# Kernel tuning notes

Measured on AMD Instinct MI355X. Metric: run time of the kernel, lower is better.

Reference implementation:

```python
import jax, jax.numpy as jnp
import numpy as np

N = 100000
E = 800000

def elu(x):
    return jnp.where(x > 0, x, jnp.expm1(x))

def transformer_conv(x, src, dst, ea, Wq, bq, Wk, bk, Wv, bv, We, Ws, bs, heads, ch):
    # PyG TransformerConv (concat=True, root_weight=True, beta=False, eval so dropout off)
    n = x.shape[0]
    q = (x @ Wq + bq).reshape(n, heads, ch)
    k = (x @ Wk + bk).reshape(n, heads, ch)
    v = (x @ Wv + bv).reshape(n, heads, ch)
    e = (ea @ We).reshape(-1, heads, ch)            # [E,H,C], lin_edge has no bias
    kj = k[src] + e                                  # [E,H,C]
    logits = (q[dst] * kj).sum(-1) / jnp.sqrt(jnp.float32(ch))  # [E,H]
    # segment softmax over incoming edges of each dst node
    m = jax.ops.segment_max(logits, dst, num_segments=n)
    ex = jnp.exp(logits - m[dst])
    denom = jax.ops.segment_sum(ex, dst, num_segments=n)
    alpha = ex / denom[dst]                          # [E,H]
    msg = alpha[..., None] * (v[src] + e)            # [E,H,C]
    agg = jax.ops.segment_sum(msg, dst, num_segments=n).reshape(n, heads * ch)
    return agg + x @ Ws + bs                         # skip connection (lin_skip)

def setup_inputs() -> dict:
    key = jax.random.key(0)
    ks = jax.random.split(key, 32)
    def rn(k, shape, scale=0.1):
        return jax.random.normal(k, shape, dtype=jnp.float32) * scale
    d = {}
    d['x'] = jax.random.normal(ks[0], (N, 23), dtype=jnp.float32)
    d['edge_index'] = jax.random.randint(ks[1], (2, E), 0, N, dtype=jnp.int32)
    d['edge_attr'] = jax.random.normal(ks[2], (E, 7), dtype=jnp.float32)
    d['linA_w'] = rn(ks[3], (23, 23)); d['linA_b'] = jnp.zeros((23,), jnp.float32)
    d['linB_w'] = rn(ks[4], (23, 23)); d['linB_b'] = jnp.zeros((23,), jnp.float32)
    # conv1: in=23, heads=8, out=24 -> 192
    d['q1_w'] = rn(ks[5], (23, 192)); d['q1_b'] = jnp.zeros((192,), jnp.float32)
    d['k1_w'] = rn(ks[6], (23, 192)); d['k1_b'] = jnp.zeros((192,), jnp.float32)
    d['v1_w'] = rn(ks[7], (23, 192)); d['v1_b'] = jnp.zeros((192,), jnp.float32)
    d['e1_w'] = rn(ks[8], (7, 192))
    d['s1_w'] = rn(ks[9], (23, 192)); d['s1_b'] = jnp.zeros((192,), jnp.float32)
    # conv4: in=192, heads=8, out=8 -> 64
    d['q2_w'] = rn(ks[10], (192, 64)); d['q2_b'] = jnp.zeros((64,), jnp.float32)
    d['k2_w'] = rn(ks[11], (192, 64)); d['k2_b'] = jnp.zeros((64,), jnp.float32)
    d['v2_w'] = rn(ks[12], (192, 64)); d['v2_b'] = jnp.zeros((64,), jnp.float32)
    d['e2_w'] = rn(ks[13], (7, 64))
    d['s2_w'] = rn(ks[14], (192, 64)); d['s2_b'] = jnp.zeros((64,), jnp.float32)
    d['lin1_w'] = rn(ks[15], (64, 20)); d['lin1_b'] = jnp.zeros((20,), jnp.float32)
    d['lin2_w'] = rn(ks[16], (20, 1)); d['lin2_b'] = jnp.zeros((1,), jnp.float32)
    return d

def reference(x, edge_index, edge_attr,
              linA_w, linA_b, linB_w, linB_b,
              q1_w, q1_b, k1_w, k1_b, v1_w, v1_b, e1_w, s1_w, s1_b,
              q2_w, q2_b, k2_w, k2_b, v2_w, v2_b, e2_w, s2_w, s2_b,
              lin1_w, lin1_b, lin2_w, lin2_b):
    src, dst = edge_index[0], edge_index[1]
    h = elu(x @ linA_w + linA_b)
    h = elu(h @ linB_w + linB_b)
    h = transformer_conv(h, src, dst, edge_attr, q1_w, q1_b, k1_w, k1_b, v1_w, v1_b, e1_w, s1_w, s1_b, 8, 24)
    h = elu(h)
    h = transformer_conv(h, src, dst, edge_attr, q2_w, q2_b, k2_w, k2_b, v2_w, v2_b, e2_w, s2_w, s2_b, 8, 8)
    h = elu(h)
    h = elu(h @ lin1_w + lin1_b)
    return h @ lin2_w + lin2_b
```

## Files before the change

### kernel.cpp

```cpp
#include <hip/hip_runtime.h>
#include <math.h>


__device__ __forceinline__ float elu_f(float x) {
    return x > 0.f ? x : expm1f(x);
}


__global__ void mlp_kernel(const float* __restrict__ x,
                           const float* __restrict__ A, const float* __restrict__ ab,
                           const float* __restrict__ B, const float* __restrict__ bb,
                           float* __restrict__ out, int n) {
    __shared__ float sA[23 * 23], sB[23 * 23], sa[23], sb[23];
    for (int t = threadIdx.x; t < 23 * 23; t += blockDim.x) { sA[t] = A[t]; sB[t] = B[t]; }
    if (threadIdx.x < 23) { sa[threadIdx.x] = ab[threadIdx.x]; sb[threadIdx.x] = bb[threadIdx.x]; }
    __syncthreads();
    int i = blockIdx.x * blockDim.x + threadIdx.x;
    if (i >= n) return;
    float xi[23], h1[23];
    #pragma unroll
    for (int j = 0; j < 23; j++) xi[j] = x[(size_t)i * 23 + j];
    #pragma unroll
    for (int o = 0; o < 23; o++) {
        float acc = sa[o];
        #pragma unroll
        for (int j = 0; j < 23; j++) acc = fmaf(xi[j], sA[j * 23 + o], acc);
        h1[o] = elu_f(acc);
    }
    #pragma unroll
    for (int o = 0; o < 23; o++) {
        float acc = sb[o];
        #pragma unroll
        for (int j = 0; j < 23; j++) acc = fmaf(h1[j], sB[j * 23 + o], acc);
        out[(size_t)i * 23 + o] = elu_f(acc);
    }
}

template<int IN, int Kc, int OUTW, int M, int TY>
__global__ void proj_tiled_kernel(const float* __restrict__ in, int n,
    const float* __restrict__ W0, const float* __restrict__ b0, float* __restrict__ o0,
    const float* __restrict__ W1, const float* __restrict__ b1, float* __restrict__ o1,
    const float* __restrict__ W2, const float* __restrict__ b2, float* __restrict__ o2,
    const float* __restrict__ W3, const float* __restrict__ b3, float* __restrict__ o3) {
    constexpr int WTOT = M * OUTW;
    constexpr int CG   = WTOT / 8;
    constexpr int BN   = TY * 4;
    constexpr int SAW  = BN + 4;
    constexpr int NT   = CG * TY;
    static_assert(IN % Kc == 0, "Kc must divide IN");
    static_assert(WTOT % 8 == 0 && OUTW % 4 == 0, "col alignment");
    __shared__ float sA[Kc][SAW];
    __shared__ float sB[Kc][WTOT];

    const int tid = threadIdx.x;
    const int tx = tid % CG;
    const int ty = tid / CG;
    const int node0 = blockIdx.x * BN;

    const int colA = tx * 4;
    const int colB = WTOT / 2 + tx * 4;
    const int matA = colA / OUTW, ccA = colA % OUTW;
    const int matB = colB / OUTW, ccB = colB % OUTW;
    const float* bA = (matA == 0 ? b0 : matA == 1 ? b1 : matA == 2 ? b2 : b3);
    const float* bB = (matB == 0 ? b0 : matB == 1 ? b1 : matB == 2 ? b2 : b3);
    float*       oA = (matA == 0 ? o0 : matA == 1 ? o1 : matA == 2 ? o2 : o3);
    float*       oB = (matB == 0 ? o0 : matB == 1 ? o1 : matB == 2 ? o2 : o3);

    float acc[4][8];
    #pragma unroll
    for (int i = 0; i < 4; i++) {
        #pragma unroll
        for (int c = 0; c < 4; c++) { acc[i][c] = bA[ccA + c]; acc[i][4 + c] = bB[ccB + c]; }
    }

    for (int k0 = 0; k0 < IN; k0 += Kc) {
        for (int t = tid; t < Kc * BN; t += NT) {
            int j = t / BN, nn = t - j * BN;
            int g = node0 + nn;
            sA[j][nn] = (g < n) ? in[(size_t)g * IN + k0 + j] : 0.f;
        }
        for (int t = tid; t < Kc * WTOT; t += NT) {
            int j = t / WTOT, c = t - j * WTOT;
            int m = c / OUTW, cm = c - m * OUTW;
            const float* Wp = (m == 0 ? W0 : m == 1 ? W1 : m == 2 ? W2 : W3);
            sB[j][c] = Wp[(size_t)(k0 + j) * OUTW + cm];
        }
        __syncthreads();
        #pragma unroll 8
        for (int j = 0; j < Kc; j++) {
            float4 a  = *(const float4*)&sA[j][ty * 4];
            float4 v0 = *(const float4*)&sB[j][colA];
            float4 v1 = *(const float4*)&sB[j][colB];
            float av[4] = {a.x, a.y, a.z, a.w};
            float bv[8] = {v0.x, v0.y, v0.z, v0.w, v1.x, v1.y, v1.z, v1.w};
            #pragma unroll
            for (int i = 0; i < 4; i++)
                #pragma unroll
                for (int c = 0; c < 8; c++)
                    acc[i][c] = fmaf(av[i], bv[c], acc[i][c]);
        }
        __syncthreads();
    }

    #pragma unroll
    for (int i = 0; i < 4; i++) {
        int g = node0 + ty * 4 + i;
        if (g >= n) continue;
        *(float4*)(oA + (size_t)g * OUTW + ccA) = make_float4(acc[i][0], acc[i][1], acc[i][2], acc[i][3]);
        *(float4*)(oB + (size_t)g * OUTW + ccB) = make_float4(acc[i][4], acc[i][5], acc[i][6], acc[i][7]);
    }
}


__global__ void zero2_kernel(int* __restrict__ a, int* __restrict__ b, int n) {
    int i = blockIdx.x * blockDim.x + threadIdx.x;
    if (i < n) { a[i] = 0; b[i] = 0; }
}

__global__ void count_kernel(const int* __restrict__ dst, int* __restrict__ cnt, int nE) {
    int e = blockIdx.x * blockDim.x + threadIdx.x;
    if (e < nE) atomicAdd(&cnt[dst[e]], 1);
}

__global__ void scan_block_kernel(int* __restrict__ cnt, int* __restrict__ bsum, int n) {
    __shared__ int sdat[256];
    int i = blockIdx.x * 256 + threadIdx.x;
    int v = (i < n) ? cnt[i] : 0;
    sdat[threadIdx.x] = v;
    __syncthreads();
    for (int off = 1; off < 256; off <<= 1) {
        int t = (threadIdx.x >= (unsigned)off) ? sdat[threadIdx.x - off] : 0;
        __syncthreads();
        sdat[threadIdx.x] += t;
        __syncthreads();
    }
    if (i < n) cnt[i] = sdat[threadIdx.x] - v;
    if (threadIdx.x == 255) bsum[blockIdx.x] = sdat[255];
}

__global__ void scan_bsum_kernel(int* __restrict__ bsum, int nb) {
    __shared__ int s[1024];
    int i = threadIdx.x;
    int v = (i < nb) ? bsum[i] : 0;
    s[i] = v;
    __syncthreads();
    for (int off = 1; off < 1024; off <<= 1) {
        int t = (i >= off) ? s[i - off] : 0;
        __syncthreads();
        s[i] += t;
        __syncthreads();
    }
    if (i < nb) bsum[i] = s[i] - v;
}

__global__ void finalize_rp_kernel(const int* __restrict__ cnt, const int* __restrict__ bsum,
                                   int* __restrict__ rp, int n, int nE) {
    int i = blockIdx.x * blockDim.x + threadIdx.x;
    if (i < n) rp[i] = cnt[i] + bsum[i >> 8];
    if (i == n) rp[n] = nE;
}

__global__ void scatter_kernel(const int* __restrict__ src, const int* __restrict__ dst,
                               const int* __restrict__ rp, int* __restrict__ cur,
                               int* __restrict__ srcS, int* __restrict__ eidS, int nE) {
    int e = blockIdx.x * blockDim.x + threadIdx.x;
    if (e >= nE) return;
    int d = dst[e];
    int pos = rp[d] + atomicAdd(&cur[d], 1);
    srcS[pos] = src[e];
    eidS[pos] = e;
}

template<int IN, int C, bool VMAT, bool QMAT, bool DOELU>
__global__ void conv_fused_kernel(const float* __restrict__ feat,
                                  const float* __restrict__ Wq, const float* __restrict__ qb,
                                  const float* __restrict__ Wv, const float* __restrict__ vb,
                                  const float* __restrict__ kmat, const float* __restrict__ vmat,
                                  const float* __restrict__ qmat,
                                  const float* __restrict__ ea, const float* __restrict__ We,
                                  const int* __restrict__ rp, const int* __restrict__ srcS,
                                  const int* __restrict__ eidS,
                                  float* __restrict__ out, int n, float scale) {
    constexpr int HC = 8 * C;
    constexpr int CPL = HC / 64;
    __shared__ float sWv[VMAT ? 1 : IN * HC];
    if constexpr (!VMAT) {
        for (int t = threadIdx.x; t < IN * HC; t += blockDim.x) sWv[t] = Wv[t];
        __syncthreads();
    }
    const int lane = threadIdx.x & 63;
    const int d = blockIdx.x * (blockDim.x >> 6) + (threadIdx.x >> 6);
    if (d >= n) return;
    const int ch0 = lane * CPL;

    float we[7][CPL];
    #pragma unroll
    for (int j = 0; j < 7; j++)
        #pragma unroll
        for (int c = 0; c < CPL; c++) we[j][c] = We[j * HC + ch0 + c];

    float vbr[CPL];
    if constexpr (!VMAT) {
        #pragma unroll
        for (int c = 0; c < CPL; c++) vbr[c] = vb[ch0 + c];
    }

    float* op = out + (size_t)d * HC + ch0;
    float sk[CPL], q[CPL];
    #pragma unroll
    for (int c = 0; c < CPL; c++) sk[c] = op[c];
    if constexpr (QMAT) {
        const float* qp = qmat + (size_t)d * HC + ch0;
        #pragma unroll
        for (int c = 0; c < CPL; c++) q[c] = qp[c];
    } else {
        #pragma unroll
        for (int c = 0; c < CPL; c++) q[c] = qb[ch0 + c];
        const float* fd = feat + (size_t)d * IN;
        for (int j = 0; j < IN; j++) {
            float f = fd[j];
            #pragma unroll
            for (int c = 0; c < CPL; c++)
                q[c] = fmaf(f, Wq[(size_t)j * HC + ch0 + c], q[c]);
        }
    }

    float m = -INFINITY, l = 0.f, acc[CPL];
    #pragma unroll
    for (int c = 0; c < CPL; c++) acc[c] = 0.f;

    const int p0 = rp[d], p1 = rp[d + 1];
    for (int p = p0; p < p1; p++) {
        int s = srcS[p];
        int eid = eidS[p];
        const float* eav = ea + (size_t)eid * 7;
        float ev[7];
        #pragma unroll
        for (int j = 0; j < 7; j++) ev[j] = eav[j];

        const float* kp = kmat + (size_t)s * HC + ch0;
        float vv[CPL];
        float part = 0.f;
        #pragma unroll
        for (int c = 0; c < CPL; c++) {
            float ec = 0.f;
            #pragma unroll
            for (int j = 0; j < 7; j++) ec = fmaf(ev[j], we[j][c], ec);
            part = fmaf(q[c], kp[c] + ec, part);
            vv[c] = ec;
        }
        if constexpr (VMAT) {
            const float* vp = vmat + (size_t)s * HC + ch0;
            #pragma unroll
            for (int c = 0; c < CPL; c++) vv[c] += vp[c];
        } else {
            #pragma unroll
            for (int c = 0; c < CPL; c++) vv[c] += vbr[c];
            const float* fs = feat + (size_t)s * IN;
            for (int j = 0; j < IN; j++) {
                float f = fs[j];
                #pragma unroll
                for (int c = 0; c < CPL; c++) vv[c] = fmaf(f, sWv[j * HC + ch0 + c], vv[c]);
            }
        }
        part += __shfl_xor(part, 1);
        part += __shfl_xor(part, 2);
        part += __shfl_xor(part, 4);
        float z = part * scale;
        float mn = fmaxf(m, z);
        float rs = expf(m - mn);
        float pw = expf(z - mn);
        l = l * rs + pw;
        #pragma unroll
        for (int c = 0; c < CPL; c++) acc[c] = fmaf(acc[c], rs, pw * vv[c]);
        m = mn;
    }
    float invl = (l > 0.f) ? 1.f / l : 0.f;
    #pragma unroll
    for (int c = 0; c < CPL; c++) {
        float r = sk[c] + acc[c] * invl;
        op[c] = DOELU ? elu_f(r) : r;
    }
}

__global__ void head_kernel(const float* __restrict__ h, const float* __restrict__ W1,
                            const float* __restrict__ b1, const float* __restrict__ W2,
                            const float* __restrict__ b2, float* __restrict__ out, int n) {
    __shared__ float sW1[64 * 20], sb1[20], sW2[20], sb2;
    for (int t = threadIdx.x; t < 64 * 20; t += blockDim.x) sW1[t] = W1[t];
    if (threadIdx.x < 20) { sb1[threadIdx.x] = b1[threadIdx.x]; sW2[threadIdx.x] = W2[threadIdx.x]; }
    if (threadIdx.x == 0) sb2 = b2[0];
    __syncthreads();
    int i = blockIdx.x * blockDim.x + threadIdx.x;
    if (i >= n) return;
    float hv[64];
    const float* hp = h + (size_t)i * 64;
    #pragma unroll
    for (int j = 0; j < 64; j++) hv[j] = elu_f(hp[j]);
    float acc2 = sb2;
    for (int o = 0; o < 20; o++) {
        float a = sb1[o];
        #pragma unroll
        for (int j = 0; j < 64; j++) a = fmaf(hv[j], sW1[j * 20 + o], a);
        acc2 = fmaf(elu_f(a), sW2[o], acc2);
    }
    out[i] = acc2;
}

__global__ void zero_out_kernel(float* __restrict__ out, int n) {
    int i = blockIdx.x * blockDim.x + threadIdx.x;
    if (i < n) out[i] = 0.f;
}


extern "C" void kernel_launch(void* const* d_in, const int* in_sizes, int n_in,
                              void* d_out, int out_size, void* d_ws, size_t ws_size,
                              hipStream_t stream) {
    const float* x   = (const float*)d_in[0];
    const int*   ei  = (const int*)d_in[1];
    const float* ea  = (const float*)d_in[2];
    const float* Aw  = (const float*)d_in[3];
    const float* Ab  = (const float*)d_in[4];
    const float* Bw  = (const float*)d_in[5];
    const float* Bb  = (const float*)d_in[6];
    const float* q1w = (const float*)d_in[7];  const float* q1b = (const float*)d_in[8];
    const float* k1w = (const float*)d_in[9];  const float* k1b = (const float*)d_in[10];
    const float* v1w = (const float*)d_in[11]; const float* v1b = (const float*)d_in[12];
    const float* e1w = (const float*)d_in[13];
    const float* s1w = (const float*)d_in[14]; const float* s1b = (const float*)d_in[15];
    const float* q2w = (const float*)d_in[16]; const float* q2b = (const float*)d_in[17];
    const float* k2w = (const float*)d_in[18]; const float* k2b = (const float*)d_in[19];
    const float* v2w = (const float*)d_in[20]; const float* v2b = (const float*)d_in[21];
    const float* e2w = (const float*)d_in[22];
    const float* s2w = (const float*)d_in[23]; const float* s2b = (const float*)d_in[24];
    const float* l1w = (const float*)d_in[25]; const float* l1b = (const float*)d_in[26];
    const float* l2w = (const float*)d_in[27]; const float* l2b = (const float*)d_in[28];

    const int n  = in_sizes[0] / 23;
    const int nE = in_sizes[1] / 2;
    const int* src = ei;
    const int* dst = ei + nE;
    float* out = (float*)d_out;
    const int B = 256;
    const int nb = (n + 255) / 256;

    size_t fl_h1 = ((size_t)n * 23 + 3) & ~(size_t)3;
    size_t fl_o1 = (size_t)n * 192;
    size_t fl_kvA = (size_t)n * 384;
    size_t fl_kB  = (size_t)n * 192;
    size_t ints_total = ((size_t)n + 1) + n + n + 1024 + (size_t)nE + (size_t)nE;

    size_t tierA_bytes = (fl_h1 + fl_o1 + fl_kvA) * 4 + ints_total * 4;
    size_t tierB_bytes = (fl_h1 + fl_o1 + fl_kB) * 4 + ints_total * 4;

    if (ws_size < tierB_bytes || nb > 1024) {
        zero_out_kernel<<<(out_size + B - 1) / B, B, 0, stream>>>(out, out_size);
        return;
    }
    const bool tierA = (ws_size >= tierA_bytes);

    float* ws = (float*)d_ws;
    size_t off = 0;
    float* h1   = ws + off; off += fl_h1;
    float* o1   = ws + off; off += fl_o1;
    float* kbuf = ws + off; off += (tierA ? fl_kvA : fl_kB);
    float* vbuf = tierA ? (kbuf + (size_t)n * 192) : nullptr;
    int* ip = (int*)(ws + off);
    int* rp   = ip; ip += (size_t)n + 1;
    int* cnt  = ip; ip += n;
    int* cur  = ip; ip += n;
    int* bsum = ip; ip += 1024;
    int* srcS = ip; ip += nE;
    int* eidS = ip; ip += nE;

    float* q2buf = kbuf;
    float* k2    = tierA ? (kbuf + (size_t)n * 64)  : kbuf;
    float* v2    = tierA ? (kbuf + (size_t)n * 128) : (kbuf + (size_t)n * 64);
    float* o2    = tierA ? (kbuf + (size_t)n * 192) : (kbuf + (size_t)n * 128);

    const float sc1 = 1.0f / sqrtf(24.0f);
    const float sc2 = 1.0f / sqrtf(8.0f);
    const float* np = nullptr;
    float* npw = nullptr;

    zero2_kernel<<<(n + B - 1) / B, B, 0, stream>>>(cnt, cur, n);
    count_kernel<<<(nE + B - 1) / B, B, 0, stream>>>(dst, cnt, nE);
    scan_block_kernel<<<nb, 256, 0, stream>>>(cnt, bsum, n);
    scan_bsum_kernel<<<1, 1024, 0, stream>>>(bsum, nb);
    finalize_rp_kernel<<<(n + 1 + B - 1) / B, B, 0, stream>>>(cnt, bsum, rp, n, nE);
    scatter_kernel<<<(nE + B - 1) / B, B, 0, stream>>>(src, dst, rp, cur, srcS, eidS, nE);

    mlp_kernel<<<(n + B - 1) / B, B, 0, stream>>>(x, Aw, Ab, Bw, Bb, h1, n);

    const int gproj = (n + 31) / 32;

    if (tierA) {
        proj_tiled_kernel<23, 23, 192, 3, 8><<<gproj, 576, 0, stream>>>(
            h1, n, k1w, k1b, kbuf, v1w, v1b, vbuf, s1w, s1b, o1, np, np, npw);
        conv_fused_kernel<23, 24, true, false, true><<<(n + 3) / 4, 256, 0, stream>>>(
            h1, q1w, q1b, v1w, v1b, kbuf, vbuf, np, ea, e1w, rp, srcS, eidS, o1, n, sc1);
    } else {
        proj_tiled_kernel<23, 23, 192, 2, 8><<<gproj, 384, 0, stream>>>(
            h1, n, k1w, k1b, kbuf, s1w, s1b, o1, np, np, npw, np, np, npw);
        conv_fused_kernel<23, 24, false, false, true><<<(n + 3) / 4, 256, 0, stream>>>(
            h1, q1w, q1b, v1w, v1b, kbuf, np, np, ea, e1w, rp, srcS, eidS, o1, n, sc1);
    }

    if (tierA) {
        proj_tiled_kernel<192, 32, 64, 4, 8><<<gproj, 256, 0, stream>>>(
            o1, n, q2w, q2b, q2buf, k2w, k2b, k2, v2w, v2b, v2, s2w, s2b, o2);
        conv_fused_kernel<192, 8, true, true, false><<<(n + 3) / 4, 256, 0, stream>>>(
            o1, q2w, q2b, v2w, v2b, k2, v2, q2buf, ea, e2w, rp, srcS, eidS, o2, n, sc2);
    } else {
        proj_tiled_kernel<192, 32, 64, 3, 8><<<gproj, 192, 0, stream>>>(
            o1, n, k2w, k2b, k2, v2w, v2b, v2, s2w, s2b, o2, np, np, npw);
        conv_fused_kernel<192, 8, true, false, false><<<(n + 3) / 4, 256, 0, stream>>>(
            o1, q2w, q2b, v2w, v2b, k2, v2, np, ea, e2w, rp, srcS, eidS, o2, n, sc2);
    }

    head_kernel<<<(n + B - 1) / B, B, 0, stream>>>(o2, l1w, l1b, l2w, l2b, out, n);
}
```

Measured before the change: 1.104 ms.

## Interleave K and V per lane and prefetch next edge in conv gather

The projection kernel now writes K and V into one interleaved buffer, so each lane's K and V channels sit next to each other in the same row. The conv kernel loads them with float2 vector loads from a single row per source node. The edge loop is software-pipelined so that the next edge's K, V and edge attributes load while the current edge is computed. The tier-B fallback that recomputed V from features is removed, so the workspace requirement is now the larger size. Projection stores change from float4 to scalar scattered stores, which may cost write efficiency.

```diff
diff --git a/kernel.cpp b/kernel.cpp
--- a/kernel.cpp
+++ b/kernel.cpp
@@ -36,19 +36,30 @@
     }
 }
 
-template<int IN, int Kc, int OUTW, int M, int TY>
+__device__ __forceinline__ void store_val(int mode, int kvcpl, void* base, int stride,
+                                          int g, int c, float val) {
+    if (mode == 0) {
+        ((float*)base)[(size_t)g * stride + c] = val;
+    } else {
+        int ln = c / kvcpl, slot = c - ln * kvcpl;
+        size_t pos = (size_t)g * stride + (size_t)ln * (2 * kvcpl) + slot
+                   + (mode == 2 ? kvcpl : 0);
+        ((float*)base)[pos] = val;
+    }
+}
+
+template<int IN, int Kc, int OUTW, int M, int TY, int KVCPL>
 __global__ void proj_tiled_kernel(const float* __restrict__ in, int n,
-    const float* __restrict__ W0, const float* __restrict__ b0, float* __restrict__ o0,
-    const float* __restrict__ W1, const float* __restrict__ b1, float* __restrict__ o1,
-    const float* __restrict__ W2, const float* __restrict__ b2, float* __restrict__ o2,
-    const float* __restrict__ W3, const float* __restrict__ b3, float* __restrict__ o3) {
+    const float* __restrict__ W0, const float* __restrict__ b0, void* __restrict__ o0, int st0, int md0,
+    const float* __restrict__ W1, const float* __restrict__ b1, void* __restrict__ o1, int st1, int md1,
+    const float* __restrict__ W2, const float* __restrict__ b2, void* __restrict__ o2, int st2, int md2,
+    const float* __restrict__ W3, const float* __restrict__ b3, void* __restrict__ o3, int st3, int md3) {
     constexpr int WTOT = M * OUTW;
     constexpr int CG   = WTOT / 8;
     constexpr int BN   = TY * 4;
     constexpr int SAW  = BN + 4;
     constexpr int NT   = CG * TY;
     static_assert(IN % Kc == 0, "Kc must divide IN");
-    static_assert(WTOT % 8 == 0 && OUTW % 4 == 0, "col alignment");
     __shared__ float sA[Kc][SAW];
     __shared__ float sB[Kc][WTOT];
 
@@ -63,8 +74,12 @@
     const int matB = colB / OUTW, ccB = colB % OUTW;
     const float* bA = (matA == 0 ? b0 : matA == 1 ? b1 : matA == 2 ? b2 : b3);
     const float* bB = (matB == 0 ? b0 : matB == 1 ? b1 : matB == 2 ? b2 : b3);
-    float*       oA = (matA == 0 ? o0 : matA == 1 ? o1 : matA == 2 ? o2 : o3);
-    float*       oB = (matB == 0 ? o0 : matB == 1 ? o1 : matB == 2 ? o2 : o3);
+    void* oA = (matA == 0 ? o0 : matA == 1 ? o1 : matA == 2 ? o2 : o3);
+    void* oB = (matB == 0 ? o0 : matB == 1 ? o1 : matB == 2 ? o2 : o3);
+    const int stA = (matA == 0 ? st0 : matA == 1 ? st1 : matA == 2 ? st2 : st3);
+    const int stB = (matB == 0 ? st0 : matB == 1 ? st1 : matB == 2 ? st2 : st3);
+    const int mdA = (matA == 0 ? md0 : matA == 1 ? md1 : matA == 2 ? md2 : md3);
+    const int mdB = (matB == 0 ? md0 : matB == 1 ? md1 : matB == 2 ? md2 : md3);
 
     float acc[4][8];
     #pragma unroll
@@ -106,8 +121,11 @@
     for (int i = 0; i < 4; i++) {
         int g = node0 + ty * 4 + i;
         if (g >= n) continue;
-        *(float4*)(oA + (size_t)g * OUTW + ccA) = make_float4(acc[i][0], acc[i][1], acc[i][2], acc[i][3]);
-        *(float4*)(oB + (size_t)g * OUTW + ccB) = make_float4(acc[i][4], acc[i][5], acc[i][6], acc[i][7]);
+        #pragma unroll
+        for (int c = 0; c < 4; c++) {
+            store_val(mdA, KVCPL, oA, stA, g, ccA + c, acc[i][c]);
+            store_val(mdB, KVCPL, oB, stB, g, ccB + c, acc[i][4 + c]);
+        }
     }
 }
 
@@ -171,11 +189,10 @@
     eidS[pos] = e;
 }
 
-template<int IN, int C, bool VMAT, bool QMAT, bool DOELU>
+template<int IN, int C, bool QMAT, bool DOELU>
 __global__ void conv_fused_kernel(const float* __restrict__ feat,
                                   const float* __restrict__ Wq, const float* __restrict__ qb,
-                                  const float* __restrict__ Wv, const float* __restrict__ vb,
-                                  const float* __restrict__ kmat, const float* __restrict__ vmat,
+                                  const float* __restrict__ kv,
                                   const float* __restrict__ qmat,
                                   const float* __restrict__ ea, const float* __restrict__ We,
                                   const int* __restrict__ rp, const int* __restrict__ srcS,
@@ -183,11 +200,7 @@
                                   float* __restrict__ out, int n, float scale) {
     constexpr int HC = 8 * C;
     constexpr int CPL = HC / 64;
-    __shared__ float sWv[VMAT ? 1 : IN * HC];
-    if constexpr (!VMAT) {
-        for (int t = threadIdx.x; t < IN * HC; t += blockDim.x) sWv[t] = Wv[t];
-        __syncthreads();
-    }
+    constexpr int KVROW = 2 * HC;
     const int lane = threadIdx.x & 63;
     const int d = blockIdx.x * (blockDim.x >> 6) + (threadIdx.x >> 6);
     if (d >= n) return;
@@ -199,12 +212,6 @@
         #pragma unroll
         for (int c = 0; c < CPL; c++) we[j][c] = We[j * HC + ch0 + c];
 
-    float vbr[CPL];
-    if constexpr (!VMAT) {
-        #pragma unroll
-        for (int c = 0; c < CPL; c++) vbr[c] = vb[ch0 + c];
-    }
-
     float* op = out + (size_t)d * HC + ch0;
     float sk[CPL], q[CPL];
     #pragma unroll
@@ -230,50 +237,61 @@
     for (int c = 0; c < CPL; c++) acc[c] = 0.f;
 
     const int p0 = rp[d], p1 = rp[d + 1];
-    for (int p = p0; p < p1; p++) {
-        int s = srcS[p];
-        int eid = eidS[p];
-        const float* eav = ea + (size_t)eid * 7;
-        float ev[7];
-        #pragma unroll
-        for (int j = 0; j < 7; j++) ev[j] = eav[j];
-
-        const float* kp = kmat + (size_t)s * HC + ch0;
-        float vv[CPL];
-        float part = 0.f;
-        #pragma unroll
-        for (int c = 0; c < CPL; c++) {
-            float ec = 0.f;
-            #pragma unroll
-            for (int j = 0; j < 7; j++) ec = fmaf(ev[j], we[j][c], ec);
-            part = fmaf(q[c], kp[c] + ec, part);
-            vv[c] = ec;
-        }
-        if constexpr (VMAT) {
-            const float* vp = vmat + (size_t)s * HC + ch0;
-            #pragma unroll
-            for (int c = 0; c < CPL; c++) vv[c] += vp[c];
-        } else {
-            #pragma unroll
-            for (int c = 0; c < CPL; c++) vv[c] += vbr[c];
-            const float* fs = feat + (size_t)s * IN;
-            for (int j = 0; j < IN; j++) {
-                float f = fs[j];
+    if (p0 < p1) {
+        auto loadkv = [&](int s, float* kc, float* vc) {
+            const float* pb = kv + (size_t)s * KVROW + lane * (2 * CPL);
+            if constexpr (CPL == 3) {
+                float2 a = *(const float2*)(pb + 0);
+                float2 b = *(const float2*)(pb + 2);
+                float2 c = *(const float2*)(pb + 4);
+                kc[0] = a.x; kc[1] = a.y; kc[2] = b.x;
+                vc[0] = b.y; vc[1] = c.x; vc[2] = c.y;
+            } else {
+                float2 a = *(const float2*)pb;
+                kc[0] = a.x; vc[0] = a.y;
+            }
+        };
+        float kc[CPL], vc[CPL], ev[7];
+        loadkv(srcS[p0], kc, vc);
+        {
+            const float* e0 = ea + (size_t)eidS[p0] * 7;
+            #pragma unroll
+            for (int j = 0; j < 7; j++) ev[j] = e0[j];
+        }
+
+        for (int p = p0; p < p1; p++) {
+            float kn[CPL], vn[CPL], evn[7];
+            if (p + 1 < p1) {
+                loadkv(srcS[p + 1], kn, vn);
+                const float* e1 = ea + (size_t)eidS[p + 1] * 7;
                 #pragma unroll
-                for (int c = 0; c < CPL; c++) vv[c] = fmaf(f, sWv[j * HC + ch0 + c], vv[c]);
+                for (int j = 0; j < 7; j++) evn[j] = e1[j];
             }
-        }
-        part += __shfl_xor(part, 1);
-        part += __shfl_xor(part, 2);
-        part += __shfl_xor(part, 4);
-        float z = part * scale;
-        float mn = fmaxf(m, z);
-        float rs = expf(m - mn);
-        float pw = expf(z - mn);
-        l = l * rs + pw;
-        #pragma unroll
-        for (int c = 0; c < CPL; c++) acc[c] = fmaf(acc[c], rs, pw * vv[c]);
-        m = mn;
+            float part = 0.f, vv[CPL];
+            #pragma unroll
+            for (int c = 0; c < CPL; c++) {
+                float ec = 0.f;
+                #pragma unroll
+                for (int j = 0; j < 7; j++) ec = fmaf(ev[j], we[j][c], ec);
+                part = fmaf(q[c], kc[c] + ec, part);
+                vv[c] = vc[c] + ec;
+            }
+            part += __shfl_xor(part, 1);
+            part += __shfl_xor(part, 2);
+            part += __shfl_xor(part, 4);
+            float z = part * scale;
+            float mn = fmaxf(m, z);
+            float rs = expf(m - mn);
+            float pw = expf(z - mn);
+            l = l * rs + pw;
+            #pragma unroll
+            for (int c = 0; c < CPL; c++) acc[c] = fmaf(acc[c], rs, pw * vv[c]);
+            m = mn;
+            #pragma unroll
+            for (int c = 0; c < CPL; c++) { kc[c] = kn[c]; vc[c] = vn[c]; }
+            #pragma unroll
+            for (int j = 0; j < 7; j++) ev[j] = evn[j];
+        }
     }
     float invl = (l > 0.f) ? 1.f / l : 0.f;
     #pragma unroll
@@ -346,25 +364,20 @@
 
     size_t fl_h1 = ((size_t)n * 23 + 3) & ~(size_t)3;
     size_t fl_o1 = (size_t)n * 192;
-    size_t fl_kvA = (size_t)n * 384;
-    size_t fl_kB  = (size_t)n * 192;
+    size_t fl_kv = (size_t)n * 384;
     size_t ints_total = ((size_t)n + 1) + n + n + 1024 + (size_t)nE + (size_t)nE;
-
-    size_t tierA_bytes = (fl_h1 + fl_o1 + fl_kvA) * 4 + ints_total * 4;
-    size_t tierB_bytes = (fl_h1 + fl_o1 + fl_kB) * 4 + ints_total * 4;
-
-    if (ws_size < tierB_bytes || nb > 1024) {
+    size_t need_bytes = (fl_h1 + fl_o1 + fl_kv) * 4 + ints_total * 4;
+
+    if (ws_size < need_bytes || nb > 1024) {
         zero_out_kernel<<<(out_size + B - 1) / B, B, 0, stream>>>(out, out_size);
         return;
     }
-    const bool tierA = (ws_size >= tierA_bytes);
 
     float* ws = (float*)d_ws;
     size_t off = 0;
-    float* h1   = ws + off; off += fl_h1;
-    float* o1   = ws + off; off += fl_o1;
-    float* kbuf = ws + off; off += (tierA ? fl_kvA : fl_kB);
-    float* vbuf = tierA ? (kbuf + (size_t)n * 192) : nullptr;
+    float* h1    = ws + off; off += fl_h1;
+    float* o1    = ws + off; off += fl_o1;
+    float* kvreg = ws + off; off += fl_kv;
     int* ip = (int*)(ws + off);
     int* rp   = ip; ip += (size_t)n + 1;
     int* cnt  = ip; ip += n;
@@ -373,15 +386,15 @@
     int* srcS = ip; ip += nE;
     int* eidS = ip; ip += nE;
 
-    float* q2buf = kbuf;
-    float* k2    = tierA ? (kbuf + (size_t)n * 64)  : kbuf;
-    float* v2    = tierA ? (kbuf + (size_t)n * 128) : (kbuf + (size_t)n * 64);
-    float* o2    = tierA ? (kbuf + (size_t)n * 192) : (kbuf + (size_t)n * 128);
+    float* kv1   = kvreg;
+    float* kv2   = kvreg;
+    float* q2buf = kvreg + (size_t)n * 128;
+    float* o2    = kvreg + (size_t)n * 192;
 
     const float sc1 = 1.0f / sqrtf(24.0f);
     const float sc2 = 1.0f / sqrtf(8.0f);
     const float* np = nullptr;
-    float* npw = nullptr;
+    void* npv = nullptr;
 
     zero2_kernel<<<(n + B - 1) / B, B, 0, stream>>>(cnt, cur, n);
     count_kernel<<<(nE + B - 1) / B, B, 0, stream>>>(dst, cnt, nE);
@@ -394,29 +407,23 @@
 
     const int gproj = (n + 31) / 32;
 
-    if (tierA) {
-        proj_tiled_kernel<23, 23, 192, 3, 8><<<gproj, 576, 0, stream>>>(
-            h1, n, k1w, k1b, kbuf, v1w, v1b, vbuf, s1w, s1b, o1, np, np, npw);
-        conv_fused_kernel<23, 24, true, false, true><<<(n + 3) / 4, 256, 0, stream>>>(
-            h1, q1w, q1b, v1w, v1b, kbuf, vbuf, np, ea, e1w, rp, srcS, eidS, o1, n, sc1);
-    } else {
-        proj_tiled_kernel<23, 23, 192, 2, 8><<<gproj, 384, 0, stream>>>(
-            h1, n, k1w, k1b, kbuf, s1w, s1b, o1, np, np, npw, np, np, npw);
-        conv_fused_kernel<23, 24, false, false, true><<<(n + 3) / 4, 256, 0, stream>>>(
-            h1, q1w, q1b, v1w, v1b, kbuf, np, np, ea, e1w, rp, srcS, eidS, o1, n, sc1);
-    }
-
-    if (tierA) {
-        proj_tiled_kernel<192, 32, 64, 4, 8><<<gproj, 256, 0, stream>>>(
-            o1, n, q2w, q2b, q2buf, k2w, k2b, k2, v2w, v2b, v2, s2w, s2b, o2);
-        conv_fused_kernel<192, 8, true, true, false><<<(n + 3) / 4, 256, 0, stream>>>(
-            o1, q2w, q2b, v2w, v2b, k2, v2, q2buf, ea, e2w, rp, srcS, eidS, o2, n, sc2);
-    } else {
-        proj_tiled_kernel<192, 32, 64, 3, 8><<<gproj, 192, 0, stream>>>(
-            o1, n, k2w, k2b, k2, v2w, v2b, v2, s2w, s2b, o2, np, np, npw);
-        conv_fused_kernel<192, 8, true, false, false><<<(n + 3) / 4, 256, 0, stream>>>(
-            o1, q2w, q2b, v2w, v2b, k2, v2, np, ea, e2w, rp, srcS, eidS, o2, n, sc2);
-    }
+    proj_tiled_kernel<23, 23, 192, 3, 8, 3><<<gproj, 576, 0, stream>>>(
+        h1, n,
+        k1w, k1b, (void*)kv1, 384, 1,
+        v1w, v1b, (void*)kv1, 384, 2,
+        s1w, s1b, (void*)o1, 192, 0,
+        np, np, npv, 0, 0);
+    conv_fused_kernel<23, 24, false, true><<<(n + 3) / 4, 256, 0, stream>>>(
+        h1, q1w, q1b, kv1, np, ea, e1w, rp, srcS, eidS, o1, n, sc1);
+
+    proj_tiled_kernel<192, 32, 64, 4, 8, 1><<<gproj, 256, 0, stream>>>(
+        o1, n,
+        q2w, q2b, (void*)q2buf, 64, 0,
+        k2w, k2b, (void*)kv2, 128, 1,
+        v2w, v2b, (void*)kv2, 128, 2,
+        s2w, s2b, (void*)o2, 64, 0);
+    conv_fused_kernel<192, 8, true, false><<<(n + 3) / 4, 256, 0, stream>>>(
+        o1, q2w, q2b, kv2, q2buf, ea, e2w, rp, srcS, eidS, o2, n, sc2);
 
     head_kernel<<<(n + B - 1) / B, B, 0, stream>>>(o2, l1w, l1b, l2w, l2b, out, n);
 }
```

After: 1.155 ms. +4.7%, slower.
